# Kernel tuning notes

Hardware: AMD Instinct MI355X
Metric: run time of the kernel (lower is better)

The kernel has to match this reference:

```python
import jax, jax.numpy as jnp
import numpy as np

B, H, W, C = 8, 128, 128, 192
WS, SS, HEADS = 8, 4, 6
NW = (H // WS) * (W // WS)
N = WS * WS

def _rel_pos_index(ws):
    coords = np.stack(np.meshgrid(np.arange(ws), np.arange(ws), indexing='ij')).reshape(2, -1)
    rel = (coords[:, :, None] - coords[:, None, :]).transpose(1, 2, 0)
    rel[:, :, 0] += ws - 1
    rel[:, :, 1] += ws - 1
    rel[:, :, 0] *= 2 * ws - 1
    return rel.sum(-1)  # (N, N) int

REL_IDX = jnp.asarray(_rel_pos_index(WS).reshape(-1))

def setup_inputs():
    key = jax.random.key(0)
    ks = jax.random.split(key, 8)
    p = lambda k, shp: jax.random.normal(k, shp, jnp.float32) * 0.02
    # exact Swin shift mask for shift=(SS,SS)
    img = np.zeros((1, H, W, 1), np.float32)
    cnt = 0
    for hs in (slice(0, -WS), slice(-WS, -SS), slice(-SS, None)):
        for vs in (slice(0, -WS), slice(-WS, -SS), slice(-SS, None)):
            img[:, hs, vs, :] = cnt; cnt += 1
    mw = img.reshape(1, H // WS, WS, W // WS, WS, 1).transpose(0, 1, 3, 2, 4, 5).reshape(-1, N)
    diff = mw[:, None, :] - mw[:, :, None]
    mask = np.where(diff != 0, -100.0, 0.0).astype(np.float32)
    return dict(
        x=jax.random.normal(ks[0], (B, H, W, C), jnp.float32),
        mask_matrix=jnp.asarray(mask),
        norm1_g=jnp.ones((C,), jnp.float32), norm1_b=jnp.zeros((C,), jnp.float32),
        qkv_w=p(ks[1], (C, 3 * C)), qkv_b=jnp.zeros((3 * C,), jnp.float32),
        rel_bias_table=p(ks[2], ((2 * WS - 1) * (2 * WS - 1), HEADS)),
        proj_w=p(ks[3], (C, C)), proj_b=jnp.zeros((C,), jnp.float32),
        norm2_g=jnp.ones((C,), jnp.float32), norm2_b=jnp.zeros((C,), jnp.float32),
        fc1_w=p(ks[4], (C, 4 * C)), fc1_b=jnp.zeros((4 * C,), jnp.float32),
        fc2_w=p(ks[5], (4 * C, C)), fc2_b=jnp.zeros((C,), jnp.float32),
    )

def _ln(x, g, b):
    m = x.mean(-1, keepdims=True)
    v = x.var(-1, keepdims=True)
    return (x - m) * jax.lax.rsqrt(v + 1e-5) * g + b

def _window_attn(xw, mask, qkv_w, qkv_b, rel_bias_table, proj_w, proj_b):
    Bw = xw.shape[0]
    hd = C // HEADS
    scale = hd ** -0.5
    # ---- spatial window attention ----
    qkv = (xw @ qkv_w + qkv_b).reshape(Bw, N, 3, HEADS, hd).transpose(2, 0, 3, 1, 4)
    q, k, v = qkv[0], qkv[1], qkv[2]  # (Bw, heads, N, hd)
    attn = jnp.einsum('bhnd,bhmd->bhnm', q, k) * scale
    bias = rel_bias_table[REL_IDX].reshape(N, N, HEADS).transpose(2, 0, 1)
    attn = attn + bias[None]
    attn = attn.reshape(Bw // NW, NW, HEADS, N, N) + mask[None, :, None]
    attn = jax.nn.softmax(attn.reshape(Bw, HEADS, N, N), axis=-1)
    x_spatial = jnp.einsum('bhnm,bhmd->bhnd', attn, v).transpose(0, 2, 1, 3).reshape(Bw, N, C)
    # ---- Fourier-domain attention branch ----
    x2d = xw.reshape(Bw, WS, WS, C)
    xf = jnp.fft.rfftn(x2d, axes=(1, 2), norm='ortho')  # (Bw, WS, WS//2+1, C) complex
    Hf, Wf = xf.shape[1], xf.shape[2]
    Nf = Hf * Wf
    def _qkv(r):  # shared qkv linear applied to real/imag parts (bias in both)
        return (r.reshape(Bw, Nf, C) @ qkv_w + qkv_b).reshape(Bw, Nf, 3, HEADS, hd).transpose(2, 0, 3, 1, 4)
    qr, qi = _qkv(xf.real), _qkv(xf.imag)
    qf = jax.lax.complex(qr[0], qi[0])
    kf = jax.lax.complex(qr[1], qi[1])
    vf = jax.lax.complex(qr[2], qi[2])
    attn_f = jnp.einsum('bhnd,bhmd->bhnm', qf, kf) * scale  # plain transpose, no conj (matches torch)
    attn_mag = jax.nn.softmax(jnp.abs(attn_f), axis=-1)
    xf_res = jnp.einsum('bhnm,bhmd->bhnd', attn_mag.astype(jnp.complex64), vf)
    xf_res = xf_res.transpose(0, 2, 1, 3).reshape(Bw, Hf, Wf, C)
    x_four = jnp.fft.irfftn(xf_res, s=(WS, WS), axes=(1, 2), norm='ortho').reshape(Bw, N, C)
    return (x_spatial + x_four) @ proj_w + proj_b

def reference(x, mask_matrix, norm1_g, norm1_b, qkv_w, qkv_b, rel_bias_table,
              proj_w, proj_b, norm2_g, norm2_b, fc1_w, fc1_b, fc2_w, fc2_b):
    shortcut = x
    xn = _ln(x, norm1_g, norm1_b)
    # shift (H,W divisible by WS so no padding needed)
    xs = jnp.roll(xn, (-SS, -SS), axis=(1, 2))
    # window partition -> (B*nW, N, C)
    xw = xs.reshape(B, H // WS, WS, W // WS, WS, C).transpose(0, 1, 3, 2, 4, 5).reshape(-1, N, C)
    aw = _window_attn(xw, mask_matrix, qkv_w, qkv_b, rel_bias_table, proj_w, proj_b)
    # window reverse + unshift
    xs = aw.reshape(B, H // WS, W // WS, WS, WS, C).transpose(0, 1, 3, 2, 4, 5).reshape(B, H, W, C)
    xo = jnp.roll(xs, (SS, SS), axis=(1, 2))
    x1 = shortcut + xo
    y = _ln(x1, norm2_g, norm2_b)
    y = jax.nn.gelu(y @ fc1_w + fc1_b, approximate=False) @ fc2_w + fc2_b
    return x1 + y
```

## Files before the change

kernel.cpp:

```cpp
#include <hip/hip_runtime.h>
#include <hip/hip_bf16.h>
#include <math.h>

#define SSH 4
#define SCALE 0.17677669529663687f

typedef __bf16 bf16x8 __attribute__((ext_vector_type(8)));
typedef __bf16 bf16x4 __attribute__((ext_vector_type(4)));
typedef unsigned short ushort8 __attribute__((ext_vector_type(8)));
typedef float  f32x4  __attribute__((ext_vector_type(4)));

static __device__ __forceinline__ f32x4 mfma16(bf16x8 a, bf16x8 b, f32x4 c){
    return __builtin_amdgcn_mfma_f32_16x16x32_bf16(a, b, c, 0, 0, 0);
}
#define MFMA16(a,b,c) mfma16((a),(b),(c))

static __device__ __forceinline__ bf16x8 ldfrag(const __bf16* p){
    return *reinterpret_cast<const bf16x8*>(p);
}
static __device__ __forceinline__ f32x4 zero4(){
    f32x4 z; z[0]=0.f; z[1]=0.f; z[2]=0.f; z[3]=0.f; return z;
}
static __device__ __forceinline__ float gelu_fast(float x){
    float u = x*(0.7978845608f + 0.0356774081f*x*x);
    return __fdividef(x, 1.f + __expf(-2.f*u));
}

__global__ __launch_bounds__(256) void k_prep(const float* __restrict__ qkvw,
        const float* __restrict__ projw, const float* __restrict__ fc1w,
        const float* __restrict__ fc2w, __bf16* __restrict__ Wq,
        __bf16* __restrict__ Wp, __bf16* __restrict__ W1, __bf16* __restrict__ W2,
        __bf16* __restrict__ Fre, __bf16* __restrict__ Fim,
        __bf16* __restrict__ Ci,  __bf16* __restrict__ nSi){
    int i = blockIdx.x*256 + threadIdx.x;
    if (i < 110592){ int n = i/192, k = i - n*192; Wq[i] = (__bf16)qkvw[k*576 + n]; }
    if (i < 36864) { int n = i/192, k = i - n*192; Wp[i] = (__bf16)projw[k*192 + n]; }
    if (i < 147456){ int n = i/192, k = i - n*192; W1[i] = (__bf16)fc1w[k*768 + n]; }
    if (i < 147456){ int n = i/768, k = i - n*768; W2[i] = (__bf16)fc2w[k*192 + n]; }
    if (i < 3072){
        int n = i>>6, p = i&63;
        float vr = 0.f, vi = 0.f;
        if (n < 40){
            int u = n/5, v = n - u*5, r = p>>3, c = p&7;
            int k = (u*r + v*c)&7;
            float ang = (float)k * 0.78539816339744831f;
            vr = cosf(ang)*0.125f; vi = -sinf(ang)*0.125f;
        }
        Fre[i] = (__bf16)vr; Fim[i] = (__bf16)vi;
    }
    if (i < 4096){
        int p = i>>6, n = i&63;
        float vc = 0.f, vs = 0.f;
        if (n < 40){
            int u = n/5, v = n - u*5, r = p>>3, c = p&7;
            int k = (u*r + v*c)&7;
            float ang = (float)k * 0.78539816339744831f;
            float wv = (v>=1 && v<=3)? 2.f : 1.f;
            vc = wv*cosf(ang)*0.125f; vs = -wv*sinf(ang)*0.125f;
        }
        Ci[i] = (__bf16)vc; nSi[i] = (__bf16)vs;
    }
}

__global__ __launch_bounds__(256,2) void k_qkv(const float* __restrict__ x,
        const float* __restrict__ n1g, const float* __restrict__ n1b,
        const __bf16* __restrict__ Wqt, const float* __restrict__ qkv_b,
        __bf16* __restrict__ S){
    __shared__ __align__(16) __bf16 xw[64*200];
    __shared__ __align__(16) __bf16 Wt[192*72];
    __shared__ __align__(16) __bf16 Ss[64*200];
    int tid = threadIdx.x;
    int win = blockIdx.x;
    int bb = win>>8, rem = win&255, wh = rem>>4, wwi = rem&15;
    {
        int tok = tid>>2, part = tid&3;
        int r = tok>>3, c = tok&7;
        int sh = (wh*8 + r + SSH)&127, sw = (wwi*8 + c + SSH)&127;
        const float* srcp = x + (((size_t)(bb*128+sh))*128 + sw)*192 + part*48;
        float v[48];
        #pragma unroll
        for (int i=0;i<12;i++){
            float4 t4 = *reinterpret_cast<const float4*>(srcp + i*4);
            v[i*4]=t4.x; v[i*4+1]=t4.y; v[i*4+2]=t4.z; v[i*4+3]=t4.w;
        }
        float s=0.f, ss=0.f;
        #pragma unroll
        for (int i=0;i<48;i++){ s+=v[i]; ss+=v[i]*v[i]; }
        s  += __shfl_xor(s,1);  s  += __shfl_xor(s,2);
        ss += __shfl_xor(ss,1); ss += __shfl_xor(ss,2);
        float mean = s*(1.f/192.f);
        float rstd = rsqrtf(ss*(1.f/192.f) - mean*mean + 1e-5f);
        #pragma unroll
        for (int i8=0;i8<6;i8++){
            bf16x8 pk;
            #pragma unroll
            for (int j=0;j<8;j++){
                int ch = part*48 + i8*8 + j;
                pk[j] = (__bf16)((v[i8*8+j]-mean)*rstd*n1g[ch] + n1b[ch]);
            }
            *reinterpret_cast<bf16x8*>(&xw[tok*200 + part*48 + i8*8]) = pk;
        }
    }
    int lane = tid&63, w = tid>>6, lr = lane&15, lg = lane>>4;
    ushort8 wreg[6];
    auto ldW = [&](int s, ushort8* wr){
        int nc = s/3, kc = s - nc*3;
        #pragma unroll
        for (int i=0;i<6;i++){
            int e = tid + i*256;
            int j = e>>3, k8 = e&7;
            wr[i] = *reinterpret_cast<const ushort8*>(
                reinterpret_cast<const unsigned short*>(Wqt) + (size_t)(nc*192+j)*192 + kc*64 + k8*8);
        }
    };
    auto stW = [&](ushort8* wr){
        #pragma unroll
        for (int i=0;i<6;i++){
            int e = tid + i*256;
            int j = e>>3, k8 = e&7;
            *reinterpret_cast<ushort8*>(reinterpret_cast<unsigned short*>(Wt) + j*72 + k8*8) = wr[i];
        }
    };
    ldW(0, wreg);
    __syncthreads();
    stW(wreg);
    __syncthreads();
    f32x4 acc[4][3];
    #pragma unroll
    for (int m=0;m<4;m++)
        #pragma unroll
        for (int n=0;n<3;n++) acc[m][n] = zero4();
    for (int s=0; s<9; s++){
        int nc = s/3, kc = s - nc*3;
        if (s<8) ldW(s+1, wreg);
        #pragma unroll
        for (int kk=0; kk<2; kk++){
            int ko = kc*64 + kk*32 + lg*8;
            bf16x8 a[4];
            #pragma unroll
            for (int m=0;m<4;m++) a[m] = ldfrag(&xw[(16*m+lr)*200 + ko]);
            int klo = kk*32 + lg*8;
            bf16x8 bfr[3];
            #pragma unroll
            for (int n=0;n<3;n++) bfr[n] = ldfrag(&Wt[(48*w+16*n+lr)*72 + klo]);
            #pragma unroll
            for (int m=0;m<4;m++)
                #pragma unroll
                for (int n=0;n<3;n++) acc[m][n] = MFMA16(a[m], bfr[n], acc[m][n]);
        }
        if (kc==2){
            #pragma unroll
            for (int n=0;n<3;n++){
                int colL = 48*w + 16*n + lr;
                float bias = qkv_b[nc*192 + colL];
                #pragma unroll
                for (int m=0;m<4;m++)
                    #pragma unroll
                    for (int r=0;r<4;r++){
                        Ss[(16*m + 4*lg + r)*200 + colL] = (__bf16)(acc[m][n][r] + bias);
                        acc[m][n][r] = 0.f;
                    }
            }
        }
        __syncthreads();
        if (kc==2){
            #pragma unroll
            for (int i=0;i<6;i++){
                int e = tid + i*256;
                int row = e/24, c8 = e - row*24;
                *reinterpret_cast<bf16x8*>(S + (size_t)(win*64+row)*576 + nc*192 + c8*8) =
                    *reinterpret_cast<const bf16x8*>(&Ss[row*200 + c8*8]);
            }
        }
        if (s<8) stW(wreg);
        __syncthreads();
    }
}

__global__ __launch_bounds__(256,4) void k_spatial(const __bf16* __restrict__ S,
        const float* __restrict__ relt, const float* __restrict__ mask,
        __bf16* __restrict__ Bb){
    __shared__ __align__(16) __bf16 P[64*72];
    __shared__ __align__(16) __bf16 Vt[32*72];
    __shared__ float reltL[1350];
    int tid = threadIdx.x;
    int win = blockIdx.x;
    int widx = win & 255;
    int lane = tid&63, w = tid>>6, lr = lane&15, lg = lane>>4;
    for (int e=tid; e<1350; e+=256) reltL[e] = relt[e];
    float mreg[16];
    int bidx[16];
    #pragma unroll
    for (int nt=0; nt<4; nt++)
        #pragma unroll
        for (int r=0;r<4;r++){
            int row = 16*w + 4*lg + r;
            int col = 16*nt + lr;
            mreg[nt*4+r] = mask[((widx*64 + row)<<6) + col];
            int dr = (row>>3)-(col>>3)+7, dc = (row&7)-(col&7)+7;
            bidx[nt*4+r] = (dr*15+dc)*6;
        }
    const size_t sbase = (size_t)win*64*576;
    const __bf16* Sq = S + sbase;
    const __bf16* Sk = S + sbase + 192;
    const __bf16* Sv = S + sbase + 384;
    for (int h=0; h<6; h++){
        __syncthreads();
        {
            int d = tid&31, pg = tid>>5;
            const __bf16* sp = Sv + (size_t)(pg*8)*576 + h*32 + d;
            bf16x4 v0, v1;
            v0[0]=sp[0];    v0[1]=sp[576];  v0[2]=sp[1152]; v0[3]=sp[1728];
            v1[0]=sp[2304]; v1[1]=sp[2880]; v1[2]=sp[3456]; v1[3]=sp[4032];
            *reinterpret_cast<bf16x4*>(&Vt[d*72 + pg*8])   = v0;
            *reinterpret_cast<bf16x4*>(&Vt[d*72 + pg*8+4]) = v1;
        }
        __syncthreads();
        bf16x8 aq = ldfrag(Sq + (size_t)(16*w+lr)*576 + h*32 + lg*8);
        f32x4 acc[4];
        #pragma unroll
        for (int nt=0;nt<4;nt++){
            bf16x8 bk = ldfrag(Sk + (size_t)(16*nt+lr)*576 + h*32 + lg*8);
            acc[nt] = MFMA16(aq, bk, zero4());
        }
        float p[16];
        #pragma unroll
        for (int r=0;r<4;r++){
            float sc[4];
            #pragma unroll
            for (int nt=0;nt<4;nt++)
                sc[nt] = acc[nt][r]*SCALE + reltL[bidx[nt*4+r] + h] + mreg[nt*4+r];
            float mx = fmaxf(fmaxf(sc[0],sc[1]),fmaxf(sc[2],sc[3]));
            mx = fmaxf(mx, __shfl_xor(mx,1));
            mx = fmaxf(mx, __shfl_xor(mx,2));
            mx = fmaxf(mx, __shfl_xor(mx,4));
            mx = fmaxf(mx, __shfl_xor(mx,8));
            float sum = 0.f;
            #pragma unroll
            for (int nt=0;nt<4;nt++){ sc[nt] = __expf(sc[nt]-mx); sum += sc[nt]; }
            sum += __shfl_xor(sum,1);
            sum += __shfl_xor(sum,2);
            sum += __shfl_xor(sum,4);
            sum += __shfl_xor(sum,8);
            float inv = 1.f/sum;
            #pragma unroll
            for (int nt=0;nt<4;nt++) p[r*4+nt] = sc[nt]*inv;
        }
        #pragma unroll
        for (int r=0;r<4;r++)
            #pragma unroll
            for (int nt=0;nt<4;nt++)
                P[(16*w + 4*lg + r)*72 + 16*nt + lr] = (__bf16)p[r*4+nt];
        #pragma unroll
        for (int dt=0; dt<2; dt++){
            f32x4 o = zero4();
            #pragma unroll
            for (int ks=0; ks<2; ks++)
                o = MFMA16(ldfrag(&P[(16*w+lr)*72 + ks*32 + lg*8]),
                           ldfrag(&Vt[(16*dt+lr)*72 + ks*32 + lg*8]), o);
            #pragma unroll
            for (int r=0;r<4;r++){
                int row = 16*w + 4*lg + r;
                Bb[((size_t)win*64 + row)*192 + h*32 + 16*dt + lr] = (__bf16)o[r];
            }
        }
    }
}

__global__ __launch_bounds__(256,3) void k_fattn(const __bf16* __restrict__ S,
        const float* __restrict__ qkv_b,
        const __bf16* __restrict__ Fre_g, const __bf16* __restrict__ Fim_g,
        const __bf16* __restrict__ Ci_g,  const __bf16* __restrict__ nSi_g,
        __bf16* __restrict__ Bb){
    __shared__ __align__(16) unsigned char arena[51968];
    __bf16* Gq_r = (__bf16*)(arena);
    __bf16* Gqin = (__bf16*)(arena + 3840);
    __bf16* Gk_r = (__bf16*)(arena + 7680);
    __bf16* Gk_i = (__bf16*)(arena + 11520);
    __bf16* Rt_r = (__bf16*)(arena);
    __bf16* Rt_i = (__bf16*)(arena + 5632);
    __bf16* Gv_r = (__bf16*)(arena + 15360);
    __bf16* Gv_i = (__bf16*)(arena + 20992);
    __bf16* St3  = (__bf16*)(arena + 26624);
    float*  Smat = (float*) (arena + 26624);
    __bf16* P    = (__bf16*)(arena + 43520);
    int tid = threadIdx.x;
    int win = blockIdx.x / 6, h = blockIdx.x - win*6;
    int lane = tid&63, w = tid>>6, lr = lane&15, lg = lane>>4;
    bf16x4 z4; z4[0]=z4[1]=z4[2]=z4[3]=(__bf16)0.f;
    const size_t sbase = (size_t)win*64*576 + h*32;
    {
        int t2 = tid & 127;
        __bf16* A = (tid<128)? Gv_r : Gv_i;
        int row = t2>>2, c4 = (t2&3)*4;
        *reinterpret_cast<bf16x4*>(A + row*88 + 48 + c4) = z4;
    }
    {
        int d = tid&31, pg = tid>>5;
        #pragma unroll
        for (int m=0;m<3;m++){
            const __bf16* sp = S + sbase + (size_t)m*192 + (size_t)pg*8*576 + d;
            bf16x4 v0, v1;
            v0[0]=sp[0];      v0[1]=sp[576];    v0[2]=sp[1152];   v0[3]=sp[1728];
            v1[0]=sp[2304];   v1[1]=sp[2880];   v1[2]=sp[3456];   v1[3]=sp[4032];
            *reinterpret_cast<bf16x4*>(&St3[m*2816 + d*88 + pg*8])     = v0;
            *reinterpret_cast<bf16x4*>(&St3[m*2816 + d*88 + pg*8 + 4]) = v1;
        }
    }
    __syncthreads();
    for (int j=w; j<36; j+=4){
        int m = j/12, jj = j - m*12;
        int term = jj/6, r2 = jj - term*6;
        const __bf16* Stm = &St3[m*2816];
        if (m<2){
            int mt = r2>>1, nt = r2&1;
            const __bf16* Ag = (term? Fim_g : Fre_g) + (16*mt+lr)*64 + lg*8;
            f32x4 acc = zero4();
            acc = MFMA16(*reinterpret_cast<const bf16x8*>(Ag),
                         ldfrag(&Stm[(16*nt+lr)*88 + lg*8]), acc);
            acc = MFMA16(*reinterpret_cast<const bf16x8*>(Ag+32),
                         ldfrag(&Stm[(16*nt+lr)*88 + 32 + lg*8]), acc);
            int d = 16*nt + lr;
            float b = qkv_b[m*192 + h*32 + d];
            __bf16* dst = (m==0)? (term? Gqin : Gq_r) : (term? Gk_i : Gk_r);
            #pragma unroll
            for (int r=0;r<4;r++){
                int n = 16*mt + 4*lg + r;
                float val = acc[r] + ((term==0) ? ((n==0)? -7.f*b : b) : b);
                if (m==0 && term==1) val = -val;
                dst[n*40 + d] = (__bf16)val;
            }
        } else {
            int mt = r2/3, nt = r2 - mt*3;
            const __bf16* Bg = (term? Fim_g : Fre_g) + (16*nt+lr)*64 + lg*8;
            f32x4 acc = zero4();
            acc = MFMA16(ldfrag(&Stm[(16*mt+lr)*88 + lg*8]),
                         *reinterpret_cast<const bf16x8*>(Bg), acc);
            acc = MFMA16(ldfrag(&Stm[(16*mt+lr)*88 + 32 + lg*8]),
                         *reinterpret_cast<const bf16x8*>(Bg+32), acc);
            int n = 16*nt + lr;
            __bf16* dst = term? Gv_i : Gv_r;
            #pragma unroll
            for (int r=0;r<4;r++){
                int d = 16*mt + 4*lg + r;
                float b = qkv_b[2*192 + h*32 + d];
                float val = acc[r] + ((term==0) ? ((n==0)? -7.f*b : b) : b);
                dst[d*88 + n] = (__bf16)val;
            }
        }
    }
    __syncthreads();
    for (int j=w; j<9; j+=4){
        int mt = j/3, nt = j - mt*3;
        bf16x8 qr = ldfrag(&Gq_r[(16*mt+lr)*40 + lg*8]);
        bf16x8 qi = ldfrag(&Gqin[(16*mt+lr)*40 + lg*8]);
        bf16x8 kr = ldfrag(&Gk_r[(16*nt+lr)*40 + lg*8]);
        bf16x8 ki = ldfrag(&Gk_i[(16*nt+lr)*40 + lg*8]);
        f32x4 sre = MFMA16(qi, ki, zero4());
        sre = MFMA16(qr, kr, sre);
        f32x4 t1 = MFMA16(qr, ki, zero4());
        f32x4 t2 = MFMA16(qi, kr, zero4());
        #pragma unroll
        for (int r=0;r<4;r++){
            float sim = t1[r] - t2[r];
            Smat[(16*mt + 4*lg + r)*52 + 16*nt + lr] =
                SCALE * sqrtf(sre[r]*sre[r] + sim*sim);
        }
    }
    __syncthreads();
    if (tid < 160){
        int row = tid>>2, part = tid&3, e0 = part*10;
        float mx = -1e30f;
        #pragma unroll
        for (int j=0;j<10;j++) mx = fmaxf(mx, Smat[row*52 + e0 + j]);
        mx = fmaxf(mx, __shfl_xor(mx,1));
        mx = fmaxf(mx, __shfl_xor(mx,2));
        float ex[10]; float sum=0.f;
        #pragma unroll
        for (int j=0;j<10;j++){ ex[j] = __expf(Smat[row*52+e0+j]-mx); sum += ex[j]; }
        sum += __shfl_xor(sum,1);
        sum += __shfl_xor(sum,2);
        float inv = 1.f/sum;
        #pragma unroll
        for (int j=0;j<10;j++) Smat[row*52+e0+j] = ex[j]*inv;
    }
    __syncthreads();
    for (int e=tid; e<3072; e+=256){
        int row = e>>6, col = e&63;
        float v = (row<40 && col<40)? Smat[row*52+col] : 0.f;
        P[row*88+col] = (__bf16)v;
    }
    {
        int t2 = tid & 127;
        __bf16* A = (tid<128)? Rt_r : Rt_i;
        int row = t2>>2, c4 = (t2&3)*4;
        *reinterpret_cast<bf16x4*>(A + row*88 + 48 + c4) = z4;
    }
    __syncthreads();
    for (int j=w; j<12; j+=4){
        int term = j/6, r2 = j - term*6;
        int dt = r2/3, nt = r2 - dt*3;
        const __bf16* Gv = term? Gv_i : Gv_r;
        f32x4 acc = zero4();
        #pragma unroll
        for (int ks=0; ks<2; ks++)
            acc = MFMA16(ldfrag(&Gv[(16*dt+lr)*88 + ks*32 + lg*8]),
                         ldfrag(&P [(16*nt+lr)*88 + ks*32 + lg*8]), acc);
        __bf16* dst = term? Rt_i : Rt_r;
        #pragma unroll
        for (int r=0;r<4;r++)
            dst[(16*dt + 4*lg + r)*88 + 16*nt + lr] = (__bf16)acc[r];
    }
    __syncthreads();
    for (int j=w; j<8; j+=4){
        int dt = j>>2, pt = j&3;
        f32x4 acc = zero4();
        #pragma unroll
        for (int ks=0; ks<2; ks++)
            acc = MFMA16(*reinterpret_cast<const bf16x8*>(nSi_g + (16*pt+lr)*64 + ks*32 + lg*8),
                         ldfrag(&Rt_i[(16*dt+lr)*88 + ks*32 + lg*8]), acc);
        #pragma unroll
        for (int ks=0; ks<2; ks++)
            acc = MFMA16(*reinterpret_cast<const bf16x8*>(Ci_g + (16*pt+lr)*64 + ks*32 + lg*8),
                         ldfrag(&Rt_r[(16*dt+lr)*88 + ks*32 + lg*8]), acc);
        #pragma unroll
        for (int r=0;r<4;r++){
            int p = 16*pt + 4*lg + r, d = 16*dt + lr;
            size_t idx = ((size_t)win*64 + p)*192 + h*32 + d;
            Bb[idx] = (__bf16)((float)Bb[idx] + acc[r]);
        }
    }
}

__global__ __launch_bounds__(256,2) void k_ffn(const __bf16* __restrict__ Bb,
        const float* __restrict__ x, const __bf16* __restrict__ Wpt,
        const float* __restrict__ proj_b, const float* __restrict__ g2,
        const float* __restrict__ b2v, const __bf16* __restrict__ W1t,
        const float* __restrict__ fc1b, const __bf16* __restrict__ W2t,
        const float* __restrict__ fc2b, float* __restrict__ out){
    __shared__ __align__(16) __bf16 hb[64*200];
    __shared__ __align__(16) __bf16 yb[64*200];
    int tid = threadIdx.x;
    int win = blockIdx.x;
    int lane = tid&63, w = tid>>6, lr = lane&15, lg = lane>>4;
    const __bf16* Ab = Bb + (size_t)win*64*192;
    f32x4 acc[4][3];
    #pragma unroll
    for (int m=0;m<4;m++)
        #pragma unroll
        for (int n=0;n<3;n++) acc[m][n] = zero4();
    #pragma unroll
    for (int kc=0; kc<6; kc++){
        int ko = kc*32 + lg*8;
        bf16x8 a[4];
        #pragma unroll
        for (int m=0;m<4;m++) a[m] = ldfrag(Ab + (size_t)(16*m+lr)*192 + ko);
        bf16x8 bfr[3];
        #pragma unroll
        for (int n=0;n<3;n++)
            bfr[n] = ldfrag(Wpt + (size_t)(48*w + 16*n + lr)*192 + ko);
        #pragma unroll
        for (int m=0;m<4;m++)
            #pragma unroll
            for (int n=0;n<3;n++) acc[m][n] = MFMA16(a[m], bfr[n], acc[m][n]);
    }
    int bb = win>>8, rem = win&255, wh = rem>>4, wwi = rem&15;
    bf16x4 yreg[4][3];
    #pragma unroll
    for (int m=0;m<4;m++)
        #pragma unroll
        for (int r=0;r<4;r++){
            int t = 16*m + 4*lg + r;
            int p = wh*8 + (t>>3), q = wwi*8 + (t&7);
            int hh = (p+SSH)&127, w2 = (q+SSH)&127;
            size_t pixb = (((size_t)bb*128 + hh)*128 + w2)*192;
            #pragma unroll
            for (int n=0;n<3;n++){
                int col = 48*w + 16*n + lr;
                float yv = acc[m][n][r] + proj_b[col] + x[pixb + col];
                __bf16 yh = (__bf16)yv;
                yreg[m][n][r] = yh;
                yb[t*200 + col] = yh;
            }
        }
    __syncthreads();
    {
        int tok = tid>>2, part = tid&3;
        float v[48];
        #pragma unroll
        for (int i8=0;i8<6;i8++){
            bf16x8 pk = *reinterpret_cast<const bf16x8*>(&yb[tok*200 + part*48 + i8*8]);
            #pragma unroll
            for (int j=0;j<8;j++) v[i8*8+j] = (float)pk[j];
        }
        float s=0.f, ss=0.f;
        #pragma unroll
        for (int i=0;i<48;i++){ s+=v[i]; ss+=v[i]*v[i]; }
        s  += __shfl_xor(s,1);  s  += __shfl_xor(s,2);
        ss += __shfl_xor(ss,1); ss += __shfl_xor(ss,2);
        float mean = s*(1.f/192.f);
        float rstd = rsqrtf(ss*(1.f/192.f) - mean*mean + 1e-5f);
        #pragma unroll
        for (int i8=0;i8<6;i8++){
            bf16x8 pk;
            #pragma unroll
            for (int j=0;j<8;j++){
                int ch = part*48 + i8*8 + j;
                pk[j] = (__bf16)((v[i8*8+j]-mean)*rstd*g2[ch] + b2v[ch]);
            }
            *reinterpret_cast<bf16x8*>(&yb[tok*200 + part*48 + i8*8]) = pk;
        }
    }
    __syncthreads();
    f32x4 acc2[4][3];
    #pragma unroll
    for (int m=0;m<4;m++)
        #pragma unroll
        for (int n=0;n<3;n++) acc2[m][n] = zero4();
    for (int hc=0; hc<4; hc++){
        f32x4 acc1[4][3];
        #pragma unroll
        for (int m=0;m<4;m++)
            #pragma unroll
            for (int n=0;n<3;n++) acc1[m][n] = zero4();
        #pragma unroll
        for (int kc=0; kc<6; kc++){
            int ko = kc*32 + lg*8;
            bf16x8 a[4];
            #pragma unroll
            for (int m=0;m<4;m++) a[m] = ldfrag(&yb[(16*m+lr)*200 + ko]);
            bf16x8 bfr[3];
            #pragma unroll
            for (int n=0;n<3;n++)
                bfr[n] = ldfrag(W1t + (size_t)(hc*192 + 48*w + 16*n + lr)*192 + ko);
            #pragma unroll
            for (int m=0;m<4;m++)
                #pragma unroll
                for (int n=0;n<3;n++) acc1[m][n] = MFMA16(a[m], bfr[n], acc1[m][n]);
        }
        #pragma unroll
        for (int n=0;n<3;n++){
            int jcol = 48*w + 16*n + lr;
            float b1 = fc1b[hc*192 + jcol];
            #pragma unroll
            for (int m=0;m<4;m++)
                #pragma unroll
                for (int r=0;r<4;r++){
                    float xv = acc1[m][n][r] + b1;
                    hb[(16*m + 4*lg + r)*200 + jcol] = (__bf16)gelu_fast(xv);
                }
        }
        __syncthreads();
        #pragma unroll
        for (int kc=0; kc<6; kc++){
            int ko = kc*32 + lg*8;
            bf16x8 a[4];
            #pragma unroll
            for (int m=0;m<4;m++) a[m] = ldfrag(&hb[(16*m+lr)*200 + ko]);
            bf16x8 bfr[3];
            #pragma unroll
            for (int n=0;n<3;n++)
                bfr[n] = ldfrag(W2t + (size_t)(48*w + 16*n + lr)*768 + hc*192 + ko);
            #pragma unroll
            for (int m=0;m<4;m++)
                #pragma unroll
                for (int n=0;n<3;n++) acc2[m][n] = MFMA16(a[m], bfr[n], acc2[m][n]);
        }
        __syncthreads();
    }
    #pragma unroll
    for (int m=0;m<4;m++)
        #pragma unroll
        for (int r=0;r<4;r++){
            int t = 16*m + 4*lg + r;
            int p = wh*8 + (t>>3), q = wwi*8 + (t&7);
            int hh = (p+SSH)&127, w2 = (q+SSH)&127;
            size_t pixb = (((size_t)bb*128 + hh)*128 + w2)*192;
            #pragma unroll
            for (int n=0;n<3;n++){
                int col = 48*w + 16*n + lr;
                out[pixb + col] = acc2[m][n][r] + fc2b[col] + (float)yreg[m][n][r];
            }
        }
}

extern "C" void kernel_launch(void* const* d_in, const int* in_sizes, int n_in,
                              void* d_out, int out_size, void* d_ws, size_t ws_size,
                              hipStream_t stream) {
    const float* x     = (const float*)d_in[0];
    const float* mask  = (const float*)d_in[1];
    const float* n1g   = (const float*)d_in[2];
    const float* n1b   = (const float*)d_in[3];
    const float* qkvw  = (const float*)d_in[4];
    const float* qkvb  = (const float*)d_in[5];
    const float* relt  = (const float*)d_in[6];
    const float* projw = (const float*)d_in[7];
    const float* projb = (const float*)d_in[8];
    const float* n2g   = (const float*)d_in[9];
    const float* n2b   = (const float*)d_in[10];
    const float* fc1w  = (const float*)d_in[11];
    const float* fc1b  = (const float*)d_in[12];
    const float* fc2w  = (const float*)d_in[13];
    const float* fc2b  = (const float*)d_in[14];
    float* out = (float*)d_out;

    char* wsb = (char*)d_ws;
    __bf16* Sb  = (__bf16*)wsb;
    __bf16* Bb  = (__bf16*)(wsb + 150994944);
    __bf16* Wqt = (__bf16*)(wsb + 251658240);
    __bf16* Wpt = (__bf16*)(wsb + 251879424);
    __bf16* W1t = (__bf16*)(wsb + 251953152);
    __bf16* W2t = (__bf16*)(wsb + 252248064);
    __bf16* Fre = (__bf16*)(wsb + 252542976);
    __bf16* Fim = (__bf16*)(wsb + 252549120);
    __bf16* Ci  = (__bf16*)(wsb + 252555264);
    __bf16* nSi = (__bf16*)(wsb + 252563456);

    k_prep   <<<576,   256, 0, stream>>>(qkvw, projw, fc1w, fc2w, Wqt, Wpt, W1t, W2t,
                                         Fre, Fim, Ci, nSi);
    k_qkv    <<<2048,  256, 0, stream>>>(x, n1g, n1b, Wqt, qkvb, Sb);
    k_spatial<<<2048,  256, 0, stream>>>(Sb, relt, mask, Bb);
    k_fattn  <<<12288, 256, 0, stream>>>(Sb, qkvb, Fre, Fim, Ci, nSi, Bb);
    k_ffn    <<<2048,  256, 0, stream>>>(Bb, x, Wpt, projb, n2g, n2b,
                                         W1t, fc1b, W2t, fc2b, out);
}
```

Baseline: 581.2 us.

## Merge spatial and Fourier attention into one launch with separate output buffers

The spatial-attention and Fourier-attention kernels are combined into a single launch that dispatches on block index: the first 12288 blocks run Fourier attention per window-head and the last 2048 run spatial attention per window. Fourier results now go to a separate buffer, and the projection kernel adds the two bf16 buffers while loading its A fragments. This removes the Fourier kernel's read-modify-write of the spatial buffer and the dependency that serialized the two kernels, so both can share the GPU at once. It adds an extra buffer read in the FFN kernel, an extra bf16 rounding before the sum, and lowers the spatial path's occupancy hint from 4 to 3. The residual x values are also prefetched into registers before the projection GEMM.

```diff
diff --git a/kernel.cpp b/kernel.cpp
--- a/kernel.cpp
+++ b/kernel.cpp
@@ -177,262 +177,261 @@
     }
 }
 
-__global__ __launch_bounds__(256,4) void k_spatial(const __bf16* __restrict__ S,
+__global__ __launch_bounds__(256,3) void k_attn2(const __bf16* __restrict__ S,
         const float* __restrict__ relt, const float* __restrict__ mask,
-        __bf16* __restrict__ Bb){
-    __shared__ __align__(16) __bf16 P[64*72];
-    __shared__ __align__(16) __bf16 Vt[32*72];
-    __shared__ float reltL[1350];
-    int tid = threadIdx.x;
-    int win = blockIdx.x;
-    int widx = win & 255;
-    int lane = tid&63, w = tid>>6, lr = lane&15, lg = lane>>4;
-    for (int e=tid; e<1350; e+=256) reltL[e] = relt[e];
-    float mreg[16];
-    int bidx[16];
-    #pragma unroll
-    for (int nt=0; nt<4; nt++)
-        #pragma unroll
-        for (int r=0;r<4;r++){
-            int row = 16*w + 4*lg + r;
-            int col = 16*nt + lr;
-            mreg[nt*4+r] = mask[((widx*64 + row)<<6) + col];
-            int dr = (row>>3)-(col>>3)+7, dc = (row&7)-(col&7)+7;
-            bidx[nt*4+r] = (dr*15+dc)*6;
-        }
-    const size_t sbase = (size_t)win*64*576;
-    const __bf16* Sq = S + sbase;
-    const __bf16* Sk = S + sbase + 192;
-    const __bf16* Sv = S + sbase + 384;
-    for (int h=0; h<6; h++){
-        __syncthreads();
-        {
-            int d = tid&31, pg = tid>>5;
-            const __bf16* sp = Sv + (size_t)(pg*8)*576 + h*32 + d;
-            bf16x4 v0, v1;
-            v0[0]=sp[0];    v0[1]=sp[576];  v0[2]=sp[1152]; v0[3]=sp[1728];
-            v1[0]=sp[2304]; v1[1]=sp[2880]; v1[2]=sp[3456]; v1[3]=sp[4032];
-            *reinterpret_cast<bf16x4*>(&Vt[d*72 + pg*8])   = v0;
-            *reinterpret_cast<bf16x4*>(&Vt[d*72 + pg*8+4]) = v1;
-        }
-        __syncthreads();
-        bf16x8 aq = ldfrag(Sq + (size_t)(16*w+lr)*576 + h*32 + lg*8);
-        f32x4 acc[4];
-        #pragma unroll
-        for (int nt=0;nt<4;nt++){
-            bf16x8 bk = ldfrag(Sk + (size_t)(16*nt+lr)*576 + h*32 + lg*8);
-            acc[nt] = MFMA16(aq, bk, zero4());
-        }
-        float p[16];
-        #pragma unroll
-        for (int r=0;r<4;r++){
-            float sc[4];
-            #pragma unroll
-            for (int nt=0;nt<4;nt++)
-                sc[nt] = acc[nt][r]*SCALE + reltL[bidx[nt*4+r] + h] + mreg[nt*4+r];
-            float mx = fmaxf(fmaxf(sc[0],sc[1]),fmaxf(sc[2],sc[3]));
-            mx = fmaxf(mx, __shfl_xor(mx,1));
-            mx = fmaxf(mx, __shfl_xor(mx,2));
-            mx = fmaxf(mx, __shfl_xor(mx,4));
-            mx = fmaxf(mx, __shfl_xor(mx,8));
-            float sum = 0.f;
-            #pragma unroll
-            for (int nt=0;nt<4;nt++){ sc[nt] = __expf(sc[nt]-mx); sum += sc[nt]; }
-            sum += __shfl_xor(sum,1);
-            sum += __shfl_xor(sum,2);
-            sum += __shfl_xor(sum,4);
-            sum += __shfl_xor(sum,8);
-            float inv = 1.f/sum;
-            #pragma unroll
-            for (int nt=0;nt<4;nt++) p[r*4+nt] = sc[nt]*inv;
-        }
-        #pragma unroll
-        for (int r=0;r<4;r++)
-            #pragma unroll
-            for (int nt=0;nt<4;nt++)
-                P[(16*w + 4*lg + r)*72 + 16*nt + lr] = (__bf16)p[r*4+nt];
-        #pragma unroll
-        for (int dt=0; dt<2; dt++){
-            f32x4 o = zero4();
-            #pragma unroll
-            for (int ks=0; ks<2; ks++)
-                o = MFMA16(ldfrag(&P[(16*w+lr)*72 + ks*32 + lg*8]),
-                           ldfrag(&Vt[(16*dt+lr)*72 + ks*32 + lg*8]), o);
-            #pragma unroll
-            for (int r=0;r<4;r++){
-                int row = 16*w + 4*lg + r;
-                Bb[((size_t)win*64 + row)*192 + h*32 + 16*dt + lr] = (__bf16)o[r];
-            }
-        }
-    }
-}
-
-__global__ __launch_bounds__(256,3) void k_fattn(const __bf16* __restrict__ S,
         const float* __restrict__ qkv_b,
         const __bf16* __restrict__ Fre_g, const __bf16* __restrict__ Fim_g,
         const __bf16* __restrict__ Ci_g,  const __bf16* __restrict__ nSi_g,
-        __bf16* __restrict__ Bb){
+        __bf16* __restrict__ Bb, __bf16* __restrict__ Fb){
     __shared__ __align__(16) unsigned char arena[51968];
-    __bf16* Gq_r = (__bf16*)(arena);
-    __bf16* Gqin = (__bf16*)(arena + 3840);
-    __bf16* Gk_r = (__bf16*)(arena + 7680);
-    __bf16* Gk_i = (__bf16*)(arena + 11520);
-    __bf16* Rt_r = (__bf16*)(arena);
-    __bf16* Rt_i = (__bf16*)(arena + 5632);
-    __bf16* Gv_r = (__bf16*)(arena + 15360);
-    __bf16* Gv_i = (__bf16*)(arena + 20992);
-    __bf16* St3  = (__bf16*)(arena + 26624);
-    float*  Smat = (float*) (arena + 26624);
-    __bf16* P    = (__bf16*)(arena + 43520);
     int tid = threadIdx.x;
-    int win = blockIdx.x / 6, h = blockIdx.x - win*6;
+    int bid = blockIdx.x;
     int lane = tid&63, w = tid>>6, lr = lane&15, lg = lane>>4;
     bf16x4 z4; z4[0]=z4[1]=z4[2]=z4[3]=(__bf16)0.f;
-    const size_t sbase = (size_t)win*64*576 + h*32;
-    {
-        int t2 = tid & 127;
-        __bf16* A = (tid<128)? Gv_r : Gv_i;
-        int row = t2>>2, c4 = (t2&3)*4;
-        *reinterpret_cast<bf16x4*>(A + row*88 + 48 + c4) = z4;
-    }
-    {
-        int d = tid&31, pg = tid>>5;
-        #pragma unroll
-        for (int m=0;m<3;m++){
-            const __bf16* sp = S + sbase + (size_t)m*192 + (size_t)pg*8*576 + d;
-            bf16x4 v0, v1;
-            v0[0]=sp[0];      v0[1]=sp[576];    v0[2]=sp[1152];   v0[3]=sp[1728];
-            v1[0]=sp[2304];   v1[1]=sp[2880];   v1[2]=sp[3456];   v1[3]=sp[4032];
-            *reinterpret_cast<bf16x4*>(&St3[m*2816 + d*88 + pg*8])     = v0;
-            *reinterpret_cast<bf16x4*>(&St3[m*2816 + d*88 + pg*8 + 4]) = v1;
-        }
-    }
-    __syncthreads();
-    for (int j=w; j<36; j+=4){
-        int m = j/12, jj = j - m*12;
-        int term = jj/6, r2 = jj - term*6;
-        const __bf16* Stm = &St3[m*2816];
-        if (m<2){
-            int mt = r2>>1, nt = r2&1;
-            const __bf16* Ag = (term? Fim_g : Fre_g) + (16*mt+lr)*64 + lg*8;
+    if (bid < 12288){
+        __bf16* Gq_r = (__bf16*)(arena);
+        __bf16* Gqin = (__bf16*)(arena + 3840);
+        __bf16* Gk_r = (__bf16*)(arena + 7680);
+        __bf16* Gk_i = (__bf16*)(arena + 11520);
+        __bf16* Rt_r = (__bf16*)(arena);
+        __bf16* Rt_i = (__bf16*)(arena + 5632);
+        __bf16* Gv_r = (__bf16*)(arena + 15360);
+        __bf16* Gv_i = (__bf16*)(arena + 20992);
+        __bf16* St3  = (__bf16*)(arena + 26624);
+        float*  Smat = (float*) (arena + 26624);
+        __bf16* P    = (__bf16*)(arena + 43520);
+        int win = bid / 6, h = bid - win*6;
+        const size_t sbase = (size_t)win*64*576 + h*32;
+        {
+            int t2 = tid & 127;
+            __bf16* A = (tid<128)? Gv_r : Gv_i;
+            int row = t2>>2, c4 = (t2&3)*4;
+            *reinterpret_cast<bf16x4*>(A + row*88 + 48 + c4) = z4;
+        }
+        {
+            int d = tid&31, pg = tid>>5;
+            #pragma unroll
+            for (int m=0;m<3;m++){
+                const __bf16* sp = S + sbase + (size_t)m*192 + (size_t)pg*8*576 + d;
+                bf16x4 v0, v1;
+                v0[0]=sp[0];      v0[1]=sp[576];    v0[2]=sp[1152];   v0[3]=sp[1728];
+                v1[0]=sp[2304];   v1[1]=sp[2880];   v1[2]=sp[3456];   v1[3]=sp[4032];
+                *reinterpret_cast<bf16x4*>(&St3[m*2816 + d*88 + pg*8])     = v0;
+                *reinterpret_cast<bf16x4*>(&St3[m*2816 + d*88 + pg*8 + 4]) = v1;
+            }
+        }
+        __syncthreads();
+        for (int j=w; j<36; j+=4){
+            int m = j/12, jj = j - m*12;
+            int term = jj/6, r2 = jj - term*6;
+            const __bf16* Stm = &St3[m*2816];
+            if (m<2){
+                int mt = r2>>1, nt = r2&1;
+                const __bf16* Ag = (term? Fim_g : Fre_g) + (16*mt+lr)*64 + lg*8;
+                f32x4 acc = zero4();
+                acc = MFMA16(*reinterpret_cast<const bf16x8*>(Ag),
+                             ldfrag(&Stm[(16*nt+lr)*88 + lg*8]), acc);
+                acc = MFMA16(*reinterpret_cast<const bf16x8*>(Ag+32),
+                             ldfrag(&Stm[(16*nt+lr)*88 + 32 + lg*8]), acc);
+                int d = 16*nt + lr;
+                float b = qkv_b[m*192 + h*32 + d];
+                __bf16* dst = (m==0)? (term? Gqin : Gq_r) : (term? Gk_i : Gk_r);
+                #pragma unroll
+                for (int r=0;r<4;r++){
+                    int n = 16*mt + 4*lg + r;
+                    float val = acc[r] + ((term==0) ? ((n==0)? -7.f*b : b) : b);
+                    if (m==0 && term==1) val = -val;
+                    dst[n*40 + d] = (__bf16)val;
+                }
+            } else {
+                int mt = r2/3, nt = r2 - mt*3;
+                const __bf16* Bg = (term? Fim_g : Fre_g) + (16*nt+lr)*64 + lg*8;
+                f32x4 acc = zero4();
+                acc = MFMA16(ldfrag(&Stm[(16*mt+lr)*88 + lg*8]),
+                             *reinterpret_cast<const bf16x8*>(Bg), acc);
+                acc = MFMA16(ldfrag(&Stm[(16*mt+lr)*88 + 32 + lg*8]),
+                             *reinterpret_cast<const bf16x8*>(Bg+32), acc);
+                int n = 16*nt + lr;
+                __bf16* dst = term? Gv_i : Gv_r;
+                #pragma unroll
+                for (int r=0;r<4;r++){
+                    int d = 16*mt + 4*lg + r;
+                    float b = qkv_b[2*192 + h*32 + d];
+                    float val = acc[r] + ((term==0) ? ((n==0)? -7.f*b : b) : b);
+                    dst[d*88 + n] = (__bf16)val;
+                }
+            }
+        }
+        __syncthreads();
+        for (int j=w; j<9; j+=4){
+            int mt = j/3, nt = j - mt*3;
+            bf16x8 qr = ldfrag(&Gq_r[(16*mt+lr)*40 + lg*8]);
+            bf16x8 qi = ldfrag(&Gqin[(16*mt+lr)*40 + lg*8]);
+            bf16x8 kr = ldfrag(&Gk_r[(16*nt+lr)*40 + lg*8]);
+            bf16x8 ki = ldfrag(&Gk_i[(16*nt+lr)*40 + lg*8]);
+            f32x4 sre = MFMA16(qi, ki, zero4());
+            sre = MFMA16(qr, kr, sre);
+            f32x4 t1 = MFMA16(qr, ki, zero4());
+            f32x4 t2 = MFMA16(qi, kr, zero4());
+            #pragma unroll
+            for (int r=0;r<4;r++){
+                float sim = t1[r] - t2[r];
+                Smat[(16*mt + 4*lg + r)*52 + 16*nt + lr] =
+                    SCALE * sqrtf(sre[r]*sre[r] + sim*sim);
+            }
+        }
+        __syncthreads();
+        if (tid < 160){
+            int row = tid>>2, part = tid&3, e0 = part*10;
+            float mx = -1e30f;
+            #pragma unroll
+            for (int j=0;j<10;j++) mx = fmaxf(mx, Smat[row*52 + e0 + j]);
+            mx = fmaxf(mx, __shfl_xor(mx,1));
+            mx = fmaxf(mx, __shfl_xor(mx,2));
+            float ex[10]; float sum=0.f;
+            #pragma unroll
+            for (int j=0;j<10;j++){ ex[j] = __expf(Smat[row*52+e0+j]-mx); sum += ex[j]; }
+            sum += __shfl_xor(sum,1);
+            sum += __shfl_xor(sum,2);
+            float inv = 1.f/sum;
+            #pragma unroll
+            for (int j=0;j<10;j++) Smat[row*52+e0+j] = ex[j]*inv;
+        }
+        __syncthreads();
+        for (int e=tid; e<3072; e+=256){
+            int row = e>>6, col = e&63;
+            float v = (row<40 && col<40)? Smat[row*52+col] : 0.f;
+            P[row*88+col] = (__bf16)v;
+        }
+        {
+            int t2 = tid & 127;
+            __bf16* A = (tid<128)? Rt_r : Rt_i;
+            int row = t2>>2, c4 = (t2&3)*4;
+            *reinterpret_cast<bf16x4*>(A + row*88 + 48 + c4) = z4;
+        }
+        __syncthreads();
+        for (int j=w; j<12; j+=4){
+            int term = j/6, r2 = j - term*6;
+            int dt = r2/3, nt = r2 - dt*3;
+            const __bf16* Gv = term? Gv_i : Gv_r;
             f32x4 acc = zero4();
-            acc = MFMA16(*reinterpret_cast<const bf16x8*>(Ag),
-                         ldfrag(&Stm[(16*nt+lr)*88 + lg*8]), acc);
-            acc = MFMA16(*reinterpret_cast<const bf16x8*>(Ag+32),
-                         ldfrag(&Stm[(16*nt+lr)*88 + 32 + lg*8]), acc);
-            int d = 16*nt + lr;
-            float b = qkv_b[m*192 + h*32 + d];
-            __bf16* dst = (m==0)? (term? Gqin : Gq_r) : (term? Gk_i : Gk_r);
+            #pragma unroll
+            for (int ks=0; ks<2; ks++)
+                acc = MFMA16(ldfrag(&Gv[(16*dt+lr)*88 + ks*32 + lg*8]),
+                             ldfrag(&P [(16*nt+lr)*88 + ks*32 + lg*8]), acc);
+            __bf16* dst = term? Rt_i : Rt_r;
+            #pragma unroll
+            for (int r=0;r<4;r++)
+                dst[(16*dt + 4*lg + r)*88 + 16*nt + lr] = (__bf16)acc[r];
+        }
+        __syncthreads();
+        for (int j=w; j<8; j+=4){
+            int dt = j>>2, pt = j&3;
+            f32x4 acc = zero4();
+            #pragma unroll
+            for (int ks=0; ks<2; ks++)
+                acc = MFMA16(*reinterpret_cast<const bf16x8*>(nSi_g + (16*pt+lr)*64 + ks*32 + lg*8),
+                             ldfrag(&Rt_i[(16*dt+lr)*88 + ks*32 + lg*8]), acc);
+            #pragma unroll
+            for (int ks=0; ks<2; ks++)
+                acc = MFMA16(*reinterpret_cast<const bf16x8*>(Ci_g + (16*pt+lr)*64 + ks*32 + lg*8),
+                             ldfrag(&Rt_r[(16*dt+lr)*88 + ks*32 + lg*8]), acc);
             #pragma unroll
             for (int r=0;r<4;r++){
-                int n = 16*mt + 4*lg + r;
-                float val = acc[r] + ((term==0) ? ((n==0)? -7.f*b : b) : b);
-                if (m==0 && term==1) val = -val;
-                dst[n*40 + d] = (__bf16)val;
-            }
-        } else {
-            int mt = r2/3, nt = r2 - mt*3;
-            const __bf16* Bg = (term? Fim_g : Fre_g) + (16*nt+lr)*64 + lg*8;
-            f32x4 acc = zero4();
-            acc = MFMA16(ldfrag(&Stm[(16*mt+lr)*88 + lg*8]),
-                         *reinterpret_cast<const bf16x8*>(Bg), acc);
-            acc = MFMA16(ldfrag(&Stm[(16*mt+lr)*88 + 32 + lg*8]),
-                         *reinterpret_cast<const bf16x8*>(Bg+32), acc);
-            int n = 16*nt + lr;
-            __bf16* dst = term? Gv_i : Gv_r;
+                int p = 16*pt + 4*lg + r, d = 16*dt + lr;
+                size_t idx = ((size_t)win*64 + p)*192 + h*32 + d;
+                Fb[idx] = (__bf16)acc[r];
+            }
+        }
+    } else {
+        float*  reltL = (float*) arena;
+        __bf16* P     = (__bf16*)(arena + 5408);
+        __bf16* Vt    = (__bf16*)(arena + 14624);
+        int win = bid - 12288;
+        int widx = win & 255;
+        for (int e=tid; e<1350; e+=256) reltL[e] = relt[e];
+        float mreg[16];
+        int bidx[16];
+        #pragma unroll
+        for (int nt=0; nt<4; nt++)
             #pragma unroll
             for (int r=0;r<4;r++){
-                int d = 16*mt + 4*lg + r;
-                float b = qkv_b[2*192 + h*32 + d];
-                float val = acc[r] + ((term==0) ? ((n==0)? -7.f*b : b) : b);
-                dst[d*88 + n] = (__bf16)val;
-            }
-        }
-    }
-    __syncthreads();
-    for (int j=w; j<9; j+=4){
-        int mt = j/3, nt = j - mt*3;
-        bf16x8 qr = ldfrag(&Gq_r[(16*mt+lr)*40 + lg*8]);
-        bf16x8 qi = ldfrag(&Gqin[(16*mt+lr)*40 + lg*8]);
-        bf16x8 kr = ldfrag(&Gk_r[(16*nt+lr)*40 + lg*8]);
-        bf16x8 ki = ldfrag(&Gk_i[(16*nt+lr)*40 + lg*8]);
-        f32x4 sre = MFMA16(qi, ki, zero4());
-        sre = MFMA16(qr, kr, sre);
-        f32x4 t1 = MFMA16(qr, ki, zero4());
-        f32x4 t2 = MFMA16(qi, kr, zero4());
-        #pragma unroll
-        for (int r=0;r<4;r++){
-            float sim = t1[r] - t2[r];
-            Smat[(16*mt + 4*lg + r)*52 + 16*nt + lr] =
-                SCALE * sqrtf(sre[r]*sre[r] + sim*sim);
-        }
-    }
-    __syncthreads();
-    if (tid < 160){
-        int row = tid>>2, part = tid&3, e0 = part*10;
-        float mx = -1e30f;
-        #pragma unroll
-        for (int j=0;j<10;j++) mx = fmaxf(mx, Smat[row*52 + e0 + j]);
-        mx = fmaxf(mx, __shfl_xor(mx,1));
-        mx = fmaxf(mx, __shfl_xor(mx,2));
-        float ex[10]; float sum=0.f;
-        #pragma unroll
-        for (int j=0;j<10;j++){ ex[j] = __expf(Smat[row*52+e0+j]-mx); sum += ex[j]; }
-        sum += __shfl_xor(sum,1);
-        sum += __shfl_xor(sum,2);
-        float inv = 1.f/sum;
-        #pragma unroll
-        for (int j=0;j<10;j++) Smat[row*52+e0+j] = ex[j]*inv;
-    }
-    __syncthreads();
-    for (int e=tid; e<3072; e+=256){
-        int row = e>>6, col = e&63;
-        float v = (row<40 && col<40)? Smat[row*52+col] : 0.f;
-        P[row*88+col] = (__bf16)v;
-    }
-    {
-        int t2 = tid & 127;
-        __bf16* A = (tid<128)? Rt_r : Rt_i;
-        int row = t2>>2, c4 = (t2&3)*4;
-        *reinterpret_cast<bf16x4*>(A + row*88 + 48 + c4) = z4;
-    }
-    __syncthreads();
-    for (int j=w; j<12; j+=4){
-        int term = j/6, r2 = j - term*6;
-        int dt = r2/3, nt = r2 - dt*3;
-        const __bf16* Gv = term? Gv_i : Gv_r;
-        f32x4 acc = zero4();
-        #pragma unroll
-        for (int ks=0; ks<2; ks++)
-            acc = MFMA16(ldfrag(&Gv[(16*dt+lr)*88 + ks*32 + lg*8]),
-                         ldfrag(&P [(16*nt+lr)*88 + ks*32 + lg*8]), acc);
-        __bf16* dst = term? Rt_i : Rt_r;
-        #pragma unroll
-        for (int r=0;r<4;r++)
-            dst[(16*dt + 4*lg + r)*88 + 16*nt + lr] = (__bf16)acc[r];
-    }
-    __syncthreads();
-    for (int j=w; j<8; j+=4){
-        int dt = j>>2, pt = j&3;
-        f32x4 acc = zero4();
-        #pragma unroll
-        for (int ks=0; ks<2; ks++)
-            acc = MFMA16(*reinterpret_cast<const bf16x8*>(nSi_g + (16*pt+lr)*64 + ks*32 + lg*8),
-                         ldfrag(&Rt_i[(16*dt+lr)*88 + ks*32 + lg*8]), acc);
-        #pragma unroll
-        for (int ks=0; ks<2; ks++)
-            acc = MFMA16(*reinterpret_cast<const bf16x8*>(Ci_g + (16*pt+lr)*64 + ks*32 + lg*8),
-                         ldfrag(&Rt_r[(16*dt+lr)*88 + ks*32 + lg*8]), acc);
-        #pragma unroll
-        for (int r=0;r<4;r++){
-            int p = 16*pt + 4*lg + r, d = 16*dt + lr;
-            size_t idx = ((size_t)win*64 + p)*192 + h*32 + d;
-            Bb[idx] = (__bf16)((float)Bb[idx] + acc[r]);
+                int row = 16*w + 4*lg + r;
+                int col = 16*nt + lr;
+                mreg[nt*4+r] = mask[((widx*64 + row)<<6) + col];
+                int dr = (row>>3)-(col>>3)+7, dc = (row&7)-(col&7)+7;
+                bidx[nt*4+r] = (dr*15+dc)*6;
+            }
+        const size_t sbase = (size_t)win*64*576;
+        const __bf16* Sq = S + sbase;
+        const __bf16* Sk = S + sbase + 192;
+        const __bf16* Sv = S + sbase + 384;
+        for (int h=0; h<6; h++){
+            __syncthreads();
+            {
+                int d = tid&31, pg = tid>>5;
+                const __bf16* sp = Sv + (size_t)(pg*8)*576 + h*32 + d;
+                bf16x4 v0, v1;
+                v0[0]=sp[0];    v0[1]=sp[576];  v0[2]=sp[1152]; v0[3]=sp[1728];
+                v1[0]=sp[2304]; v1[1]=sp[2880]; v1[2]=sp[3456]; v1[3]=sp[4032];
+                *reinterpret_cast<bf16x4*>(&Vt[d*72 + pg*8])   = v0;
+                *reinterpret_cast<bf16x4*>(&Vt[d*72 + pg*8+4]) = v1;
+            }
+            __syncthreads();
+            bf16x8 aq = ldfrag(Sq + (size_t)(16*w+lr)*576 + h*32 + lg*8);
+            f32x4 acc[4];
+            #pragma unroll
+            for (int nt=0;nt<4;nt++){
+                bf16x8 bk = ldfrag(Sk + (size_t)(16*nt+lr)*576 + h*32 + lg*8);
+                acc[nt] = MFMA16(aq, bk, zero4());
+            }
+            float p[16];
+            #pragma unroll
+            for (int r=0;r<4;r++){
+                float sc[4];
+                #pragma unroll
+                for (int nt=0;nt<4;nt++)
+                    sc[nt] = acc[nt][r]*SCALE + reltL[bidx[nt*4+r] + h] + mreg[nt*4+r];
+                float mx = fmaxf(fmaxf(sc[0],sc[1]),fmaxf(sc[2],sc[3]));
+                mx = fmaxf(mx, __shfl_xor(mx,1));
+                mx = fmaxf(mx, __shfl_xor(mx,2));
+                mx = fmaxf(mx, __shfl_xor(mx,4));
+                mx = fmaxf(mx, __shfl_xor(mx,8));
+                float sum = 0.f;
+                #pragma unroll
+                for (int nt=0;nt<4;nt++){ sc[nt] = __expf(sc[nt]-mx); sum += sc[nt]; }
+                sum += __shfl_xor(sum,1);
+                sum += __shfl_xor(sum,2);
+                sum += __shfl_xor(sum,4);
+                sum += __shfl_xor(sum,8);
+                float inv = 1.f/sum;
+                #pragma unroll
+                for (int nt=0;nt<4;nt++) p[r*4+nt] = sc[nt]*inv;
+            }
+            #pragma unroll
+            for (int r=0;r<4;r++)
+                #pragma unroll
+                for (int nt=0;nt<4;nt++)
+                    P[(16*w + 4*lg + r)*72 + 16*nt + lr] = (__bf16)p[r*4+nt];
+            #pragma unroll
+            for (int dt=0; dt<2; dt++){
+                f32x4 o = zero4();
+                #pragma unroll
+                for (int ks=0; ks<2; ks++)
+                    o = MFMA16(ldfrag(&P[(16*w+lr)*72 + ks*32 + lg*8]),
+                               ldfrag(&Vt[(16*dt+lr)*72 + ks*32 + lg*8]), o);
+                #pragma unroll
+                for (int r=0;r<4;r++){
+                    int row = 16*w + 4*lg + r;
+                    Bb[((size_t)win*64 + row)*192 + h*32 + 16*dt + lr] = (__bf16)o[r];
+                }
+            }
         }
     }
 }
 
 __global__ __launch_bounds__(256,2) void k_ffn(const __bf16* __restrict__ Bb,
+        const __bf16* __restrict__ Fb,
         const float* __restrict__ x, const __bf16* __restrict__ Wpt,
         const float* __restrict__ proj_b, const float* __restrict__ g2,
         const float* __restrict__ b2v, const __bf16* __restrict__ W1t,
@@ -443,7 +442,22 @@
     int tid = threadIdx.x;
     int win = blockIdx.x;
     int lane = tid&63, w = tid>>6, lr = lane&15, lg = lane>>4;
+    int bb = win>>8, rem = win&255, wh = rem>>4, wwi = rem&15;
+    float xr[4][4][3];
+    #pragma unroll
+    for (int m=0;m<4;m++)
+        #pragma unroll
+        for (int r=0;r<4;r++){
+            int t = 16*m + 4*lg + r;
+            int p = wh*8 + (t>>3), q = wwi*8 + (t&7);
+            int hh = (p+SSH)&127, w2 = (q+SSH)&127;
+            size_t pixb = (((size_t)bb*128 + hh)*128 + w2)*192;
+            #pragma unroll
+            for (int n=0;n<3;n++)
+                xr[m][r][n] = x[pixb + 48*w + 16*n + lr];
+        }
     const __bf16* Ab = Bb + (size_t)win*64*192;
+    const __bf16* Af = Fb + (size_t)win*64*192;
     f32x4 acc[4][3];
     #pragma unroll
     for (int m=0;m<4;m++)
@@ -454,7 +468,14 @@
         int ko = kc*32 + lg*8;
         bf16x8 a[4];
         #pragma unroll
-        for (int m=0;m<4;m++) a[m] = ldfrag(Ab + (size_t)(16*m+lr)*192 + ko);
+        for (int m=0;m<4;m++){
+            bf16x8 ab = ldfrag(Ab + (size_t)(16*m+lr)*192 + ko);
+            bf16x8 fb = ldfrag(Af + (size_t)(16*m+lr)*192 + ko);
+            bf16x8 s;
+            #pragma unroll
+            for (int j=0;j<8;j++) s[j] = (__bf16)((float)ab[j] + (float)fb[j]);
+            a[m] = s;
+        }
         bf16x8 bfr[3];
         #pragma unroll
         for (int n=0;n<3;n++)
@@ -464,20 +485,16 @@
             #pragma unroll
             for (int n=0;n<3;n++) acc[m][n] = MFMA16(a[m], bfr[n], acc[m][n]);
     }
-    int bb = win>>8, rem = win&255, wh = rem>>4, wwi = rem&15;
     bf16x4 yreg[4][3];
     #pragma unroll
     for (int m=0;m<4;m++)
         #pragma unroll
         for (int r=0;r<4;r++){
             int t = 16*m + 4*lg + r;
-            int p = wh*8 + (t>>3), q = wwi*8 + (t&7);
-            int hh = (p+SSH)&127, w2 = (q+SSH)&127;
-            size_t pixb = (((size_t)bb*128 + hh)*128 + w2)*192;
             #pragma unroll
             for (int n=0;n<3;n++){
                 int col = 48*w + 16*n + lr;
-                float yv = acc[m][n][r] + proj_b[col] + x[pixb + col];
+                float yv = acc[m][n][r] + proj_b[col] + xr[m][r][n];
                 __bf16 yh = (__bf16)yv;
                 yreg[m][n][r] = yh;
                 yb[t*200 + col] = yh;
@@ -607,6 +624,7 @@
     char* wsb = (char*)d_ws;
     __bf16* Sb  = (__bf16*)wsb;
     __bf16* Bb  = (__bf16*)(wsb + 150994944);
+    __bf16* Fb  = (__bf16*)(wsb + 201326592);
     __bf16* Wqt = (__bf16*)(wsb + 251658240);
     __bf16* Wpt = (__bf16*)(wsb + 251879424);
     __bf16* W1t = (__bf16*)(wsb + 251953152);
@@ -616,11 +634,10 @@
     __bf16* Ci  = (__bf16*)(wsb + 252555264);
     __bf16* nSi = (__bf16*)(wsb + 252563456);
 
-    k_prep   <<<576,   256, 0, stream>>>(qkvw, projw, fc1w, fc2w, Wqt, Wpt, W1t, W2t,
-                                         Fre, Fim, Ci, nSi);
-    k_qkv    <<<2048,  256, 0, stream>>>(x, n1g, n1b, Wqt, qkvb, Sb);
-    k_spatial<<<2048,  256, 0, stream>>>(Sb, relt, mask, Bb);
-    k_fattn  <<<12288, 256, 0, stream>>>(Sb, qkvb, Fre, Fim, Ci, nSi, Bb);
-    k_ffn    <<<2048,  256, 0, stream>>>(Bb, x, Wpt, projb, n2g, n2b,
-                                         W1t, fc1b, W2t, fc2b, out);
-}
+    k_prep  <<<576,   256, 0, stream>>>(qkvw, projw, fc1w, fc2w, Wqt, Wpt, W1t, W2t,
+                                        Fre, Fim, Ci, nSi);
+    k_qkv   <<<2048,  256, 0, stream>>>(x, n1g, n1b, Wqt, qkvb, Sb);
+    k_attn2 <<<14336, 256, 0, stream>>>(Sb, relt, mask, qkvb, Fre, Fim, Ci, nSi, Bb, Fb);
+    k_ffn   <<<2048,  256, 0, stream>>>(Bb, Fb, x, Wpt, projb, n2g, n2b,
+                                        W1t, fc1b, W2t, fc2b, out);
+}
```

Result: no change. 585.3 us (+0.7%).
